# Kernel optimization log

Hardware: AMD Instinct MI355X
Metric: run time of the kernel (lower is better)

The kernel has to match this reference:

```python
import jax, jax.numpy as jnp
import numpy as np

D_MODEL, D_FF, RANK = 1024, 4096, 128
BATCH, SEQ = 4, 2048


def setup_inputs() -> dict:
    key = jax.random.key(0)
    ks = jax.random.split(key, 9)
    s = 0.02  # typical transformer init scale
    return {
        "x": jax.random.normal(ks[0], (BATCH, SEQ, D_MODEL), jnp.float32),
        "cfc_U": jax.random.normal(ks[1], (D_MODEL, RANK), jnp.float32) * s,
        "cfc_S": jax.random.uniform(ks[2], (RANK,), jnp.float32, 0.5, 1.5),
        "cfc_V": jax.random.normal(ks[3], (D_FF, RANK), jnp.float32) * s,
        "cfc_bias": jax.random.normal(ks[4], (D_FF,), jnp.float32) * s,
        "cproj_U": jax.random.normal(ks[5], (D_FF, RANK), jnp.float32) * s,
        "cproj_S": jax.random.uniform(ks[6], (RANK,), jnp.float32, 0.5, 1.5),
        "cproj_V": jax.random.normal(ks[7], (D_MODEL, RANK), jnp.float32) * s,
        "cproj_bias": jax.random.normal(ks[8], (D_MODEL,), jnp.float32) * s,
    }


def reference(x, cfc_U, cfc_S, cfc_V, cfc_bias, cproj_U, cproj_S, cproj_V, cproj_bias):
    # c_fc_weight = (U * S) @ V^T  -> [d_model, d_ff];  h = x @ c_fc_weight + b
    cfc_w = (cfc_U * cfc_S[None, :]) @ cfc_V.T            # [D_MODEL, D_FF]
    h = jnp.einsum('bsd,df->bsf', x, cfc_w) + cfc_bias    # [B, S, D_FF]
    h = jax.nn.gelu(h, approximate=False)                 # nn.GELU() = exact erf
    cproj_w = (cproj_U * cproj_S[None, :]) @ cproj_V.T    # [D_FF, D_MODEL]
    out = jnp.einsum('bsf,fd->bsd', h, cproj_w) + cproj_bias
    return out
```

## Files before the change

kernel.cpp:

```cpp
#include <hip/hip_runtime.h>
#include <math.h>

#define D_MODEL 1024
#define D_FF    4096
#define RANK    128
#define M_ROWS  8192

typedef _Float16 f16;
typedef _Float16 f16x8 __attribute__((ext_vector_type(8)));
typedef float    f32x4 __attribute__((ext_vector_type(4)));

#define MFMA16(a, b, c) __builtin_amdgcn_mfma_f32_16x16x32_f16((a), (b), (c), 0, 0, 0)

__device__ __forceinline__ f16x8 ld8(const f16* p) { return *(const f16x8*)p; }

__device__ __forceinline__ f16x8 cvt8(float4 a0, float4 a1) {
    f16x8 r = { (f16)a0.x, (f16)a0.y, (f16)a0.z, (f16)a0.w,
                (f16)a1.x, (f16)a1.y, (f16)a1.z, (f16)a1.w };
    return r;
}

__device__ __forceinline__ float gelu_exact(float v) {
    return 0.5f * v * (1.0f + erff(v * 0.70710678118654752440f));
}

__global__ __launch_bounds__(256) void k_prep(
    const float* __restrict__ cfcU, const float* __restrict__ cfcS,
    const float* __restrict__ cfcV, const float* __restrict__ pjU,
    const float* __restrict__ pjS,  const float* __restrict__ pjV,
    f16* __restrict__ w1T, f16* __restrict__ v1,
    f16* __restrict__ w2T, f16* __restrict__ v2)
{
    int i = blockIdx.x * 256 + threadIdx.x;
    if (i < 131072) {
        int r = i >> 10, d = i & 1023;
        w1T[i] = (f16)(cfcU[d * RANK + r] * cfcS[r]);
    } else if (i < 655360) {
        int j = i - 131072;
        v1[j] = (f16)cfcV[j];
    } else if (i < 1179648) {
        int j = i - 655360;
        int r = j >> 12, f = j & 4095;
        w2T[j] = (f16)(pjU[f * RANK + r] * pjS[r]);
    } else if (i < 1310720) {
        int j = i - 1179648;
        v2[j] = (f16)pjV[j];
    }
}

__global__ __launch_bounds__(256, 2) void k_t1(
    const float* __restrict__ x, const f16* __restrict__ w1T,
    f16* __restrict__ t1p)
{
    __shared__ __align__(16) float xs[32 * 132];
    __shared__ __align__(16) f16   w1s[128 * 136];

    const int tid  = threadIdx.x;
    const int lane = tid & 63;
    const int wv   = tid >> 6;
    const int wm   = wv & 1, wn = wv >> 1;
    const int m0b  = blockIdx.x * 32;
    const int ks   = blockIdx.y;
    const int k0   = ks * 512;
    const int c    = lane & 15, q = lane >> 4;

    f32x4 acc[4] = {};

#pragma unroll 1
    for (int kc = 0; kc < 4; ++kc) {
        const int kbase = k0 + kc * 128;
        __syncthreads();
#pragma unroll
        for (int it = 0; it < 4; ++it) {
            int id = it * 256 + tid;
            int mm = id >> 5, k4 = id & 31;
            *(float4*)&xs[mm * 132 + k4 * 4] =
                *(const float4*)&x[(size_t)(m0b + mm) * D_MODEL + kbase + k4 * 4];
        }
#pragma unroll
        for (int it = 0; it < 8; ++it) {
            int id = it * 256 + tid;
            int nn = id >> 4, k8 = id & 15;
            *(f16x8*)&w1s[nn * 136 + k8 * 8] =
                ld8(w1T + (size_t)nn * D_MODEL + kbase + k8 * 8);
        }
        __syncthreads();

#pragma unroll
        for (int kb = 0; kb < 4; ++kb) {
            const float* ap = &xs[(wm * 16 + c) * 132 + kb * 32 + q * 8];
            f16x8 af = cvt8(*(const float4*)ap, *(const float4*)(ap + 4));
#pragma unroll
            for (int nt = 0; nt < 4; ++nt) {
                f16x8 bf = *(const f16x8*)&w1s[(wn * 64 + nt * 16 + c) * 136 + kb * 32 + q * 8];
                acc[nt] = MFMA16(af, bf, acc[nt]);
            }
        }
    }

    f16* o = t1p + (size_t)ks * (M_ROWS * RANK);
#pragma unroll
    for (int nt = 0; nt < 4; ++nt)
#pragma unroll
        for (int i2 = 0; i2 < 4; ++i2)
            o[(size_t)(m0b + wm * 16 + q * 4 + i2) * RANK + wn * 64 + nt * 16 + c] =
                (f16)acc[nt][i2];
}

#define RED_STORE(buf, acc)                                            \
    _Pragma("unroll") for (int rt = 0; rt < 8; ++rt)                   \
    _Pragma("unroll") for (int i2 = 0; i2 < 4; ++i2)                   \
        (buf)[(q * 4 + i2) * 132 + rt * 16 + c] = (acc)[rt][i2];
#define RED_ADD(buf, acc)                                              \
    _Pragma("unroll") for (int rt = 0; rt < 8; ++rt)                   \
    _Pragma("unroll") for (int i2 = 0; i2 < 4; ++i2)                   \
        (acc)[rt][i2] += (buf)[(q * 4 + i2) * 132 + rt * 16 + c];

__global__ __launch_bounds__(256, 2) void k_fused(
    const f16* __restrict__ t1p, const f16* __restrict__ v1,
    const float* __restrict__ bfc, const f16* __restrict__ w2T,
    f16* __restrict__ t2p)
{
    __shared__ __align__(16) char smem[78848];
    f16*  v1s = (f16*)smem;
    f16*  w2s = (f16*)(smem + 34816);
    f16*  hs  = (f16*)(smem + 69632);
    float* red = (float*)smem;

    const int tid  = threadIdx.x;
    const int lane = tid & 63;
    const int wv   = tid >> 6;
    const int wm   = wv & 1, wf = wv >> 1;
    const int m0b  = blockIdx.x * 32;
    const int s    = blockIdx.y;
    const int c    = lane & 15, q = lane >> 4;

    f16x8 a2[4];
#pragma unroll
    for (int kb = 0; kb < 4; ++kb) {
        const size_t off = (size_t)(m0b + wm * 16 + c) * RANK + kb * 32 + q * 8;
        f16x8 p0 = ld8(t1p + off);
        f16x8 p1 = ld8(t1p + (size_t)(M_ROWS * RANK) + off);
#pragma unroll
        for (int e = 0; e < 8; ++e)
            a2[kb][e] = (f16)((float)p0[e] + (float)p1[e]);
    }

    f32x4 c3[8] = {};

#pragma unroll 1
    for (int it = 0; it < 16; ++it) {
        const int fbase = s * 2048 + it * 128;
        __syncthreads();
#pragma unroll
        for (int i8 = 0; i8 < 8; ++i8) {
            int id = i8 * 256 + tid;
            int ff = id >> 4, r8 = id & 15;
            *(f16x8*)&v1s[ff * 136 + r8 * 8] =
                ld8(v1 + (size_t)(fbase + ff) * RANK + r8 * 8);
        }
#pragma unroll
        for (int i8 = 0; i8 < 8; ++i8) {
            int id = i8 * 256 + tid;
            int rr = id >> 4, f8 = id & 15;
            *(f16x8*)&w2s[rr * 136 + f8 * 8] =
                ld8(w2T + (size_t)rr * D_FF + fbase + f8 * 8);
        }
        __syncthreads();

        const int f0 = fbase + wf * 64;

        f32x4 c2[4] = {};
#pragma unroll
        for (int nt = 0; nt < 4; ++nt)
#pragma unroll
            for (int kb = 0; kb < 4; ++kb) {
                f16x8 bf = *(const f16x8*)
                    &v1s[(wf * 64 + nt * 16 + c) * 136 + kb * 32 + q * 8];
                c2[nt] = MFMA16(a2[kb], bf, c2[nt]);
            }

#pragma unroll
        for (int nt = 0; nt < 4; ++nt) {
            float b = bfc[f0 + nt * 16 + c];
#pragma unroll
            for (int i2 = 0; i2 < 4; ++i2)
                hs[(wv * 16 + q * 4 + i2) * 72 + nt * 16 + c] =
                    (f16)gelu_exact(c2[nt][i2] + b);
        }
        asm volatile("s_waitcnt lgkmcnt(0)" ::: "memory");

#pragma unroll
        for (int kb2 = 0; kb2 < 2; ++kb2) {
            f16x8 a3 = *(const f16x8*)&hs[(wv * 16 + c) * 72 + kb2 * 32 + q * 8];
#pragma unroll
            for (int rt = 0; rt < 8; ++rt) {
                f16x8 bf = *(const f16x8*)
                    &w2s[(rt * 16 + c) * 136 + wf * 64 + kb2 * 32 + q * 8];
                c3[rt] = MFMA16(a3, bf, c3[rt]);
            }
        }
        asm volatile("s_waitcnt lgkmcnt(0)" ::: "memory");
    }

    __syncthreads();
    if (wf == 1) { RED_STORE(&red[wm * 16 * 132], c3) }
    __syncthreads();
    if (wf == 0) {
        RED_ADD(&red[wm * 16 * 132], c3)
        f16* o = t2p + (size_t)s * (M_ROWS * RANK);
#pragma unroll
        for (int rt = 0; rt < 8; ++rt)
#pragma unroll
            for (int i2 = 0; i2 < 4; ++i2)
                o[(size_t)(m0b + wm * 16 + q * 4 + i2) * RANK + rt * 16 + c] =
                    (f16)c3[rt][i2];
    }
}

__global__ __launch_bounds__(256, 2) void k_out(
    const f16* __restrict__ t2p, const f16* __restrict__ v2,
    const float* __restrict__ bpj, float* __restrict__ out)
{
    __shared__ __align__(16) f16 v2s[256 * 136];

    const int tid  = threadIdx.x;
    const int lane = tid & 63;
    const int wv   = tid >> 6;
    const int wm   = wv & 1, wn = wv >> 1;
    const int m0b  = blockIdx.x * 32;
    const int n0b  = blockIdx.y * 256;
    const int c    = lane & 15, q = lane >> 4;

#pragma unroll
    for (int i8 = 0; i8 < 16; ++i8) {
        int id = i8 * 256 + tid;
        int nn = id >> 4, k8 = id & 15;
        *(f16x8*)&v2s[nn * 136 + k8 * 8] =
            ld8(v2 + (size_t)(n0b + nn) * RANK + k8 * 8);
    }

    f16x8 a[4];
#pragma unroll
    for (int kb = 0; kb < 4; ++kb) {
        const size_t off = (size_t)(m0b + wm * 16 + c) * RANK + kb * 32 + q * 8;
        f16x8 p0 = ld8(t2p + off);
        f16x8 p1 = ld8(t2p + (size_t)(M_ROWS * RANK) + off);
#pragma unroll
        for (int e = 0; e < 8; ++e)
            a[kb][e] = (f16)((float)p0[e] + (float)p1[e]);
    }
    __syncthreads();

    f32x4 acc[8] = {};
#pragma unroll
    for (int nt = 0; nt < 8; ++nt)
#pragma unroll
        for (int kb = 0; kb < 4; ++kb) {
            f16x8 bf = *(const f16x8*)
                &v2s[(wn * 128 + nt * 16 + c) * 136 + kb * 32 + q * 8];
            acc[nt] = MFMA16(a[kb], bf, acc[nt]);
        }

#pragma unroll
    for (int nt = 0; nt < 8; ++nt) {
        float b = bpj[n0b + wn * 128 + nt * 16 + c];
#pragma unroll
        for (int i2 = 0; i2 < 4; ++i2)
            out[(size_t)(m0b + wm * 16 + q * 4 + i2) * D_MODEL +
                n0b + wn * 128 + nt * 16 + c] = acc[nt][i2] + b;
    }
}

extern "C" void kernel_launch(void* const* d_in, const int* in_sizes, int n_in,
                              void* d_out, int out_size, void* d_ws, size_t ws_size,
                              hipStream_t stream) {
    const float* x    = (const float*)d_in[0];
    const float* cfcU = (const float*)d_in[1];
    const float* cfcS = (const float*)d_in[2];
    const float* cfcV = (const float*)d_in[3];
    const float* cfcB = (const float*)d_in[4];
    const float* pjU  = (const float*)d_in[5];
    const float* pjS  = (const float*)d_in[6];
    const float* pjV  = (const float*)d_in[7];
    const float* pjB  = (const float*)d_in[8];
    float* out = (float*)d_out;

    f16* wsf = (f16*)d_ws;
    f16* t1p = wsf;
    f16* t2p = wsf + 2097152;
    f16* w1T = wsf + 4194304;
    f16* v1  = w1T + 131072;
    f16* w2T = v1  + 524288;
    f16* v2  = w2T + 524288;

    k_prep <<<dim3(5120), 256, 0, stream>>>(cfcU, cfcS, cfcV, pjU, pjS, pjV,
                                            w1T, v1, w2T, v2);
    k_t1   <<<dim3(M_ROWS / 32, 2), 256, 0, stream>>>(x, w1T, t1p);
    k_fused<<<dim3(M_ROWS / 32, 2), 256, 0, stream>>>(t1p, v1, cfcB, w2T, t2p);
    k_out  <<<dim3(M_ROWS / 32, D_MODEL / 256), 256, 0, stream>>>(t2p, v2, pjB, out);
}
```

Before: 181.2 us.

## Double-buffer tile loads in registers and widen k_t1/k_fused to 512 threads

k_t1 now handles 64 rows per block with 512 threads. It loads the whole 512-wide K slice of w1T into LDS once, and reads x straight from global into registers with a two-deep software pipeline instead of staging it through LDS. k_fused also moves to 512 threads and 64 rows per block, with a remapped 1D grid. Its v1/w2T tiles are prefetched into registers one iteration ahead, so global latency overlaps the MFMA and GELU work. The cost is more registers and LDS per block, and only 256 blocks per kernel, which may limit latency hiding.

After: 177.6 us. Within noise of the previous version (-2.0%).

```diff
diff --git a/kernel.cpp b/kernel.cpp
--- a/kernel.cpp
+++ b/kernel.cpp
@@ -48,63 +48,65 @@
     }
 }
 
-__global__ __launch_bounds__(256, 2) void k_t1(
+__global__ __launch_bounds__(512, 2) void k_t1(
     const float* __restrict__ x, const f16* __restrict__ w1T,
     f16* __restrict__ t1p)
 {
-    __shared__ __align__(16) float xs[32 * 132];
-    __shared__ __align__(16) f16   w1s[128 * 136];
+    __shared__ __align__(16) f16 w1s[128 * 520];
 
     const int tid  = threadIdx.x;
     const int lane = tid & 63;
     const int wv   = tid >> 6;
-    const int wm   = wv & 1, wn = wv >> 1;
-    const int m0b  = blockIdx.x * 32;
-    const int ks   = blockIdx.y;
-    const int k0   = ks * 512;
+    const int wm   = wv & 3, wn = wv >> 2;
+    const int m0b  = blockIdx.x * 64;
+    const int h    = blockIdx.y;
     const int c    = lane & 15, q = lane >> 4;
 
+#define LOADX(dst, kc)                                                          \
+    _Pragma("unroll") for (int kb = 0; kb < 4; ++kb) {                          \
+        const float* px = &x[(size_t)(m0b + wm * 16 + c) * D_MODEL +            \
+                             h * 512 + (kc) * 128 + kb * 32 + q * 8];           \
+        dst[kb][0] = *(const float4*)px;                                        \
+        dst[kb][1] = *(const float4*)(px + 4); }
+
+#define COMPUTEKC(src, kc)                                                      \
+    _Pragma("unroll") for (int kb = 0; kb < 4; ++kb) {                          \
+        f16x8 af = cvt8(src[kb][0], src[kb][1]);                                \
+        _Pragma("unroll") for (int nt = 0; nt < 4; ++nt) {                      \
+            f16x8 bf = *(const f16x8*)                                          \
+                &w1s[(wn * 64 + nt * 16 + c) * 520 + (kc) * 128 + kb * 32 + q * 8]; \
+            acc[nt] = MFMA16(af, bf, acc[nt]); } }
+
+    float4 xa[4][2], xb[4][2];
+    LOADX(xa, 0)
+
+#pragma unroll
+    for (int i = 0; i < 16; ++i) {
+        int id = i * 512 + tid;
+        int rr = id >> 6, k8 = id & 63;
+        *(f16x8*)&w1s[rr * 520 + k8 * 8] =
+            ld8(w1T + (size_t)rr * D_MODEL + h * 512 + k8 * 8);
+    }
+    __syncthreads();
+
     f32x4 acc[4] = {};
-
-#pragma unroll 1
-    for (int kc = 0; kc < 4; ++kc) {
-        const int kbase = k0 + kc * 128;
-        __syncthreads();
-#pragma unroll
-        for (int it = 0; it < 4; ++it) {
-            int id = it * 256 + tid;
-            int mm = id >> 5, k4 = id & 31;
-            *(float4*)&xs[mm * 132 + k4 * 4] =
-                *(const float4*)&x[(size_t)(m0b + mm) * D_MODEL + kbase + k4 * 4];
-        }
-#pragma unroll
-        for (int it = 0; it < 8; ++it) {
-            int id = it * 256 + tid;
-            int nn = id >> 4, k8 = id & 15;
-            *(f16x8*)&w1s[nn * 136 + k8 * 8] =
-                ld8(w1T + (size_t)nn * D_MODEL + kbase + k8 * 8);
-        }
-        __syncthreads();
-
-#pragma unroll
-        for (int kb = 0; kb < 4; ++kb) {
-            const float* ap = &xs[(wm * 16 + c) * 132 + kb * 32 + q * 8];
-            f16x8 af = cvt8(*(const float4*)ap, *(const float4*)(ap + 4));
-#pragma unroll
-            for (int nt = 0; nt < 4; ++nt) {
-                f16x8 bf = *(const f16x8*)&w1s[(wn * 64 + nt * 16 + c) * 136 + kb * 32 + q * 8];
-                acc[nt] = MFMA16(af, bf, acc[nt]);
-            }
-        }
-    }
-
-    f16* o = t1p + (size_t)ks * (M_ROWS * RANK);
+    LOADX(xb, 1)
+    COMPUTEKC(xa, 0)
+    LOADX(xa, 2)
+    COMPUTEKC(xb, 1)
+    LOADX(xb, 3)
+    COMPUTEKC(xa, 2)
+    COMPUTEKC(xb, 3)
+
+    f16* o = t1p + (size_t)h * (M_ROWS * RANK);
 #pragma unroll
     for (int nt = 0; nt < 4; ++nt)
 #pragma unroll
         for (int i2 = 0; i2 < 4; ++i2)
             o[(size_t)(m0b + wm * 16 + q * 4 + i2) * RANK + wn * 64 + nt * 16 + c] =
                 (f16)acc[nt][i2];
+#undef LOADX
+#undef COMPUTEKC
 }
 
 #define RED_STORE(buf, acc)                                            \
@@ -116,12 +118,93 @@
     _Pragma("unroll") for (int i2 = 0; i2 < 4; ++i2)                   \
         (acc)[rt][i2] += (buf)[(q * 4 + i2) * 132 + rt * 16 + c];
 
-__global__ __launch_bounds__(256, 2) void k_fused(
+__device__ __forceinline__ void load_tiles(
+    const f16* __restrict__ v1, const f16* __restrict__ w2T,
+    int tid, int fb, f16x8 nv[4], f16x8 nw[4])
+{
+#pragma unroll
+    for (int i = 0; i < 4; ++i) {
+        int id = i * 512 + tid;
+        nv[i] = ld8(v1 + (size_t)(fb + (id >> 4)) * RANK + (id & 15) * 8);
+    }
+#pragma unroll
+    for (int i = 0; i < 4; ++i) {
+        int id = i * 512 + tid;
+        nw[i] = ld8(w2T + (size_t)(id >> 4) * D_FF + fb + (id & 15) * 8);
+    }
+}
+
+__device__ __forceinline__ void fused_step(
+    const f16* __restrict__ v1, const f16* __restrict__ w2T,
+    const float* __restrict__ bfc,
+    f16* v1s, f16* w2s, f16* hs,
+    const f16x8 a2[4], f32x4 c3[8],
+    f16x8 cv[4], f16x8 cw[4], f16x8 nv[4], f16x8 nw[4],
+    int tid, int s, int it, bool prefetch)
+{
+    const int lane = tid & 63;
+    const int wv   = tid >> 6;
+    const int wf   = wv >> 2;
+    const int c    = lane & 15, q = lane >> 4;
+    const int fbase = s * 2048 + it * 128;
+
+    if (prefetch)
+        load_tiles(v1, w2T, tid, fbase + 128, nv, nw);
+
+    __syncthreads();
+#pragma unroll
+    for (int i = 0; i < 4; ++i) {
+        int id = i * 512 + tid;
+        *(f16x8*)&v1s[(id >> 4) * 136 + (id & 15) * 8] = cv[i];
+    }
+#pragma unroll
+    for (int i = 0; i < 4; ++i) {
+        int id = i * 512 + tid;
+        *(f16x8*)&w2s[(id >> 4) * 136 + (id & 15) * 8] = cw[i];
+    }
+    __syncthreads();
+
+    const int f0 = fbase + wf * 64;
+
+    f32x4 c2[4] = {};
+#pragma unroll
+    for (int nt = 0; nt < 4; ++nt)
+#pragma unroll
+        for (int kb = 0; kb < 4; ++kb) {
+            f16x8 bf = *(const f16x8*)
+                &v1s[(wf * 64 + nt * 16 + c) * 136 + kb * 32 + q * 8];
+            c2[nt] = MFMA16(a2[kb], bf, c2[nt]);
+        }
+
+#pragma unroll
+    for (int nt = 0; nt < 4; ++nt) {
+        float b = bfc[f0 + nt * 16 + c];
+#pragma unroll
+        for (int i2 = 0; i2 < 4; ++i2)
+            hs[(wv * 16 + q * 4 + i2) * 72 + nt * 16 + c] =
+                (f16)gelu_exact(c2[nt][i2] + b);
+    }
+    asm volatile("s_waitcnt lgkmcnt(0)" ::: "memory");
+
+#pragma unroll
+    for (int kb2 = 0; kb2 < 2; ++kb2) {
+        f16x8 a3 = *(const f16x8*)&hs[(wv * 16 + c) * 72 + kb2 * 32 + q * 8];
+#pragma unroll
+        for (int rt = 0; rt < 8; ++rt) {
+            f16x8 bf = *(const f16x8*)
+                &w2s[(rt * 16 + c) * 136 + wf * 64 + kb2 * 32 + q * 8];
+            c3[rt] = MFMA16(a3, bf, c3[rt]);
+        }
+    }
+    asm volatile("s_waitcnt lgkmcnt(0)" ::: "memory");
+}
+
+__global__ __launch_bounds__(512, 2) void k_fused(
     const f16* __restrict__ t1p, const f16* __restrict__ v1,
     const float* __restrict__ bfc, const f16* __restrict__ w2T,
     f16* __restrict__ t2p)
 {
-    __shared__ __align__(16) char smem[78848];
+    __shared__ __align__(16) char smem[88064];
     f16*  v1s = (f16*)smem;
     f16*  w2s = (f16*)(smem + 34816);
     f16*  hs  = (f16*)(smem + 69632);
@@ -130,10 +213,13 @@
     const int tid  = threadIdx.x;
     const int lane = tid & 63;
     const int wv   = tid >> 6;
-    const int wm   = wv & 1, wf = wv >> 1;
-    const int m0b  = blockIdx.x * 32;
-    const int s    = blockIdx.y;
+    const int wm   = wv & 3, wf = wv >> 2;
     const int c    = lane & 15, q = lane >> 4;
+
+    const int bx  = blockIdx.x;
+    const int s   = (bx & 7) >> 2;
+    const int mb  = (bx >> 3) * 4 + (bx & 3);
+    const int m0b = mb * 64;
 
     f16x8 a2[4];
 #pragma unroll
@@ -146,61 +232,16 @@
             a2[kb][e] = (f16)((float)p0[e] + (float)p1[e]);
     }
 
+    f16x8 pv[4], pw[4], qv[4], qw[4];
+    load_tiles(v1, w2T, tid, s * 2048, pv, pw);
+
     f32x4 c3[8] = {};
-
 #pragma unroll 1
-    for (int it = 0; it < 16; ++it) {
-        const int fbase = s * 2048 + it * 128;
-        __syncthreads();
-#pragma unroll
-        for (int i8 = 0; i8 < 8; ++i8) {
-            int id = i8 * 256 + tid;
-            int ff = id >> 4, r8 = id & 15;
-            *(f16x8*)&v1s[ff * 136 + r8 * 8] =
-                ld8(v1 + (size_t)(fbase + ff) * RANK + r8 * 8);
-        }
-#pragma unroll
-        for (int i8 = 0; i8 < 8; ++i8) {
-            int id = i8 * 256 + tid;
-            int rr = id >> 4, f8 = id & 15;
-            *(f16x8*)&w2s[rr * 136 + f8 * 8] =
-                ld8(w2T + (size_t)rr * D_FF + fbase + f8 * 8);
-        }
-        __syncthreads();
-
-        const int f0 = fbase + wf * 64;
-
-        f32x4 c2[4] = {};
-#pragma unroll
-        for (int nt = 0; nt < 4; ++nt)
-#pragma unroll
-            for (int kb = 0; kb < 4; ++kb) {
-                f16x8 bf = *(const f16x8*)
-                    &v1s[(wf * 64 + nt * 16 + c) * 136 + kb * 32 + q * 8];
-                c2[nt] = MFMA16(a2[kb], bf, c2[nt]);
-            }
-
-#pragma unroll
-        for (int nt = 0; nt < 4; ++nt) {
-            float b = bfc[f0 + nt * 16 + c];
-#pragma unroll
-            for (int i2 = 0; i2 < 4; ++i2)
-                hs[(wv * 16 + q * 4 + i2) * 72 + nt * 16 + c] =
-                    (f16)gelu_exact(c2[nt][i2] + b);
-        }
-        asm volatile("s_waitcnt lgkmcnt(0)" ::: "memory");
-
-#pragma unroll
-        for (int kb2 = 0; kb2 < 2; ++kb2) {
-            f16x8 a3 = *(const f16x8*)&hs[(wv * 16 + c) * 72 + kb2 * 32 + q * 8];
-#pragma unroll
-            for (int rt = 0; rt < 8; ++rt) {
-                f16x8 bf = *(const f16x8*)
-                    &w2s[(rt * 16 + c) * 136 + wf * 64 + kb2 * 32 + q * 8];
-                c3[rt] = MFMA16(a3, bf, c3[rt]);
-            }
-        }
-        asm volatile("s_waitcnt lgkmcnt(0)" ::: "memory");
+    for (int it = 0; it < 16; it += 2) {
+        fused_step(v1, w2T, bfc, v1s, w2s, hs, a2, c3,
+                   pv, pw, qv, qw, tid, s, it, true);
+        fused_step(v1, w2T, bfc, v1s, w2s, hs, a2, c3,
+                   qv, qw, pv, pw, tid, s, it + 1, it + 2 < 16);
     }
 
     __syncthreads();
@@ -296,7 +337,7 @@
 
     k_prep <<<dim3(5120), 256, 0, stream>>>(cfcU, cfcS, cfcV, pjU, pjS, pjV,
                                             w1T, v1, w2T, v2);
-    k_t1   <<<dim3(M_ROWS / 32, 2), 256, 0, stream>>>(x, w1T, t1p);
-    k_fused<<<dim3(M_ROWS / 32, 2), 256, 0, stream>>>(t1p, v1, cfcB, w2T, t2p);
+    k_t1   <<<dim3(M_ROWS / 64, 2), 512, 0, stream>>>(x, w1T, t1p);
+    k_fused<<<dim3(256), 512, 0, stream>>>(t1p, v1, cfcB, w2T, t2p);
     k_out  <<<dim3(M_ROWS / 32, D_MODEL / 256), 256, 0, stream>>>(t2p, v2, pjB, out);
 }
```
